# Performance work log

Measured on AMD Instinct MI355X. Metric: run time of the kernel, lower is better.

Reference implementation:

```python
import jax, jax.numpy as jnp
import numpy as np

N = 50000      # num nodes
E = 800000     # num edges
IN_DIM = 128
OUT_DIM = 128
HEADS = 4
HEAD_DIM = OUT_DIM // HEADS  # concat=True
TAU = 1.0


def setup_inputs() -> dict:
    key = jax.random.key(0)
    ks = jax.random.split(key, 8)
    x = jax.random.normal(ks[0], (N, IN_DIM), dtype=jnp.float32)
    edge_index = jax.random.randint(ks[1], (2, E), 0, N, dtype=jnp.int64)
    # xavier-uniform-ish linear weights, stored as (in, out) so y = x @ W
    def xavier(k, fan_in, fan_out):
        limit = np.sqrt(6.0 / (fan_in + fan_out)).astype(np.float32)
        return jax.random.uniform(k, (fan_in, fan_out), jnp.float32, -limit, limit)
    Wt = xavier(ks[2], IN_DIM, HEADS * HEAD_DIM)
    Ws = xavier(ks[3], IN_DIM, HEADS * HEAD_DIM)
    Wc = xavier(ks[4], IN_DIM, HEADS * HEAD_DIM)
    Wout = xavier(ks[5], HEADS * HEAD_DIM, OUT_DIM)
    bout = jnp.zeros((OUT_DIM,), jnp.float32)
    return {"x": x, "edge_index": edge_index, "Wt": Wt, "Ws": Ws,
            "Wc": Wc, "Wout": Wout, "bout": bout}


def reference(x, edge_index, Wt, Ws, Wc, Wout, bout):
    src = edge_index[0]  # j (source of message)
    dst = edge_index[1]  # i (target, softmax group)
    q = (x @ Wt).reshape(N, HEADS, HEAD_DIM)
    k = (x @ Ws).reshape(N, HEADS, HEAD_DIM)
    v = (x @ Wc).reshape(N, HEADS, HEAD_DIM)
    # per-edge dot-product scores: (E, H)
    scores = jnp.einsum('ehd,ehd->eh', q[dst], k[src]) / TAU
    # segment softmax over incoming edges of each dst node
    m = jax.ops.segment_max(scores, dst, num_segments=N)        # (N, H)
    e = jnp.exp(scores - m[dst])                                # (E, H)
    denom = jax.ops.segment_sum(e, dst, num_segments=N)         # (N, H)
    alpha = e / denom[dst]                                      # (E, H)
    # weighted scatter-add aggregation
    msg = v[src] * alpha[:, :, None]                            # (E, H, D)
    agg = jax.ops.segment_sum(msg, dst, num_segments=N)         # (N, H, D)
    out = agg.reshape(N, HEADS * HEAD_DIM) @ Wout + bout
    out = jax.nn.relu(out)
    # residual: in_dim == out_dim -> identity projection
    return out + x
```

## Files before the change

kernel.cpp:

```cpp
#include <hip/hip_runtime.h>
#include <hip/hip_bf16.h>

#define HEADS 4
#define HEAD_DIM 32
#define SLAB 128

typedef __bf16 bf16x8 __attribute__((ext_vector_type(8)));
typedef float  f32x4  __attribute__((ext_vector_type(4)));
typedef _Float16 h2   __attribute__((ext_vector_type(2)));

__device__ __forceinline__ unsigned short f2bf(float f) {
    unsigned u = __float_as_uint(f);
    u += 0x7fffu + ((u >> 16) & 1u);
    return (unsigned short)(u >> 16);
}
__device__ __forceinline__ unsigned pack2bf(float a, float b) {
    return (unsigned)f2bf(a) | ((unsigned)f2bf(b) << 16);
}
__device__ __forceinline__ unsigned short f2h(float f) {
    _Float16 h = (_Float16)f;
    return *(unsigned short*)&h;
}

__global__ __launch_bounds__(256) void fillw_kernel(
    const float* __restrict__ W0, const float* __restrict__ W1,
    const float* __restrict__ W2, const float* __restrict__ W3,
    unsigned short* __restrict__ Wsw,
    const int* __restrict__ edge, int E,
    int* __restrict__ cnt, int* __restrict__ col)
{
    if (blockIdx.x < 32) {
        const float* Wm[4] = { W0, W1, W2, W3 };
        int mi = blockIdx.x >> 3;
        const float* __restrict__ W = Wm[mi];
        unsigned short* __restrict__ o = Wsw + (size_t)mi * 16384;
        int t = (blockIdx.x & 7) * 256 + threadIdx.x;
        int kg = t >> 7;
        int n  = t & 127;
        ushort4 p0, p1;
        p0.x = f2bf(W[(kg * 8 + 0) * 128 + n]);
        p0.y = f2bf(W[(kg * 8 + 1) * 128 + n]);
        p0.z = f2bf(W[(kg * 8 + 2) * 128 + n]);
        p0.w = f2bf(W[(kg * 8 + 3) * 128 + n]);
        p1.x = f2bf(W[(kg * 8 + 4) * 128 + n]);
        p1.y = f2bf(W[(kg * 8 + 5) * 128 + n]);
        p1.z = f2bf(W[(kg * 8 + 6) * 128 + n]);
        p1.w = f2bf(W[(kg * 8 + 7) * 128 + n]);
        *(ushort4*)(o + kg * 1024 + n * 8)     = p0;
        *(ushort4*)(o + kg * 1024 + n * 8 + 4) = p1;
    } else {
        int e = (blockIdx.x - 32) * 256 + threadIdx.x;
        if (e < E) {
            int dst = edge[E + e];
            int src = edge[e];
            int pos = atomicAdd(&cnt[dst], 1);
            if (pos < SLAB)
                col[(size_t)dst * SLAB + pos] = src;
        }
    }
}

__device__ __forceinline__ void mfma_compute64g(
    const unsigned short* As, const unsigned short* __restrict__ Bsw,
    f32x4 (&acc)[2][4], int mb, int nb, int quad, int l16)
{
    #pragma unroll
    for (int a = 0; a < 2; a++)
        #pragma unroll
        for (int b = 0; b < 4; b++)
            #pragma unroll
            for (int e = 0; e < 4; e++) acc[a][b][e] = 0.f;

    #pragma unroll
    for (int kk = 0; kk < 4; kk++) {
        bf16x8 af[2], bf[4];
        #pragma unroll
        for (int mt = 0; mt < 2; mt++)
            af[mt] = *(const bf16x8*)(As + (mb + mt * 16 + l16) * 136
                                         + kk * 32 + quad * 8);
        #pragma unroll
        for (int nt = 0; nt < 4; nt++)
            bf[nt] = *(const bf16x8*)(Bsw + (kk * 4 + quad) * 1024
                                          + (nb + nt * 16 + l16) * 8);
        #pragma unroll
        for (int mt = 0; mt < 2; mt++)
            #pragma unroll
            for (int nt = 0; nt < 4; nt++)
                acc[mt][nt] = __builtin_amdgcn_mfma_f32_16x16x32_bf16(
                    af[mt], bf[nt], acc[mt][nt], 0, 0, 0);
    }
}

__global__ __launch_bounds__(256) void qkv_kernel(
    const float* __restrict__ x, const unsigned short* __restrict__ Wsw,
    unsigned short* __restrict__ qh, unsigned short* __restrict__ kh,
    unsigned short* __restrict__ vh, int M)
{
    __shared__ __align__(16) unsigned short As[64 * 136];
    const int r0 = blockIdx.x * 64;
    const int t  = threadIdx.x;

    #pragma unroll
    for (int it = 0; it < 4; it++) {
        int c   = t + it * 256;
        int row = c >> 4, kp = c & 15;
        float4 a = make_float4(0.f, 0.f, 0.f, 0.f);
        float4 b = make_float4(0.f, 0.f, 0.f, 0.f);
        if (r0 + row < M) {
            a = *(const float4*)(x + (size_t)(r0 + row) * 128 + kp * 8);
            b = *(const float4*)(x + (size_t)(r0 + row) * 128 + kp * 8 + 4);
        }
        uint4 pk;
        pk.x = pack2bf(a.x, a.y);
        pk.y = pack2bf(a.z, a.w);
        pk.z = pack2bf(b.x, b.y);
        pk.w = pack2bf(b.z, b.w);
        *(uint4*)(As + row * 136 + kp * 8) = pk;
    }
    __syncthreads();

    const int wave = t >> 6, L = t & 63;
    const int quad = L >> 4, l16 = L & 15;
    const int mb = (wave >> 1) * 32;
    const int nb = (wave & 1) * 64;

    #pragma unroll
    for (int mode = 0; mode < 3; mode++) {
        f32x4 acc[2][4];
        mfma_compute64g(As, Wsw + (size_t)mode * 16384, acc, mb, nb, quad, l16);

        unsigned short* ob = (mode == 0) ? qh : (mode == 1) ? kh : vh;
        #pragma unroll
        for (int mt = 0; mt < 2; mt++) {
            #pragma unroll
            for (int nt = 0; nt < 4; nt++) {
                int colj = nb + nt * 16 + l16;
                #pragma unroll
                for (int r = 0; r < 4; r++) {
                    int row = r0 + mb + mt * 16 + quad * 4 + r;
                    if (row < M)
                        ob[(size_t)row * 128 + colj] = f2h(acc[mt][nt][r]);
                }
            }
        }
    }
}

__global__ __launch_bounds__(256) void out_mfma_kernel(
    const unsigned short* __restrict__ aggh, const unsigned short* __restrict__ Wsw,
    const float* __restrict__ bout, const float* __restrict__ x,
    float* __restrict__ out, int M)
{
    __shared__ __align__(16) unsigned short As[64 * 136];
    const int r0 = blockIdx.x * 64;
    const int t  = threadIdx.x;

    #pragma unroll
    for (int it = 0; it < 4; it++) {
        int c   = t + it * 256;
        int row = c >> 4, kp = c & 15;
        uint4 val = make_uint4(0, 0, 0, 0);
        if (r0 + row < M)
            val = *(const uint4*)(aggh + (size_t)(r0 + row) * 128 + kp * 8);
        *(uint4*)(As + row * 136 + kp * 8) = val;
    }
    __syncthreads();

    const int wave = t >> 6, L = t & 63;
    const int quad = L >> 4, l16 = L & 15;
    const int mb = (wave >> 1) * 32;
    const int nb = (wave & 1) * 64;

    f32x4 acc[2][4];
    mfma_compute64g(As, Wsw, acc, mb, nb, quad, l16);

    #pragma unroll
    for (int mt = 0; mt < 2; mt++) {
        #pragma unroll
        for (int nt = 0; nt < 4; nt++) {
            int colj = nb + nt * 16 + l16;
            float b = bout[colj];
            #pragma unroll
            for (int r = 0; r < 4; r++) {
                int row = r0 + mb + mt * 16 + quad * 4 + r;
                if (row < M) {
                    float val = fmaxf(acc[mt][nt][r] + b, 0.f)
                              + x[(size_t)row * 128 + colj];
                    out[(size_t)row * 128 + colj] = val;
                }
            }
        }
    }
}

__global__ __launch_bounds__(256, 8) void attn_kernel(
    const unsigned short* __restrict__ qhB, const unsigned short* __restrict__ kh,
    const unsigned short* __restrict__ vh,
    const int* __restrict__ cnt, const int* __restrict__ col,
    unsigned short* __restrict__ aggh, int N)
{
    const int wv   = threadIdx.x >> 6;
    const int lane = threadIdx.x & 63;
    const int dst  = blockIdx.x * 4 + wv;
    if (dst >= N) return;

    __shared__ __align__(16) unsigned short kbuf[4][16 * 136];
    __shared__ __align__(16) float swW[4][64];

    const size_t orow = (size_t)dst * 128;
    const size_t slab = (size_t)dst * SLAB;

    const int h    = lane & 3;
    const int eo   = lane >> 2;
    const int hv   = lane >> 4;
    const int rr   = lane >> 4;
    const int cseg = (lane & 15) * 8;

    const int degr = cnt[dst];
    const int colv = col[slab + lane];
    uint4 qreg[4];
    {
        const uint4* qp = (const uint4*)(qhB + orow + h * HEAD_DIM);
        qreg[0] = qp[0]; qreg[1] = qp[1]; qreg[2] = qp[2]; qreg[3] = qp[3];
    }
    const h2* qv = (const h2*)qreg;

    const int deg = min(degr, SLAB);
    if (deg == 0) {
        *(unsigned*)(aggh + orow + 2 * lane) = 0u;
        return;
    }
    const int srcA = (lane < deg) ? colv : 0;
    int srcB = 0;
    if (__builtin_expect(deg > 64, 0)) {
        if (64 + lane < deg) srcB = col[slab + 64 + lane];
    }

    float sreg[8];
    #pragma unroll
    for (int c = 0; c < 8; c++) {
        sreg[c] = -3.4e38f;
        if (c * 16 < deg) {
            const int nle  = deg - c * 16;
            const int csrc = (c < 4) ? srcA : srcB;
            const int lsel = (c & 3) * 16;
            #pragma unroll
            for (int i = 0; i < 4; i++) {
                int r  = i * 4 + rr;
                int sr = __shfl(csrc, lsel + r);
                uint4 kv = *(const uint4*)(kh + (size_t)sr * 128 + cseg);
                *(uint4*)(&kbuf[wv][r * 136 + cseg]) = kv;
            }
            if (eo < nle) {
                const unsigned short* kb = &kbuf[wv][eo * 136 + h * 32];
                uint4 u0 = *(const uint4*)(kb);
                uint4 u1 = *(const uint4*)(kb + 8);
                uint4 u2 = *(const uint4*)(kb + 16);
                uint4 u3 = *(const uint4*)(kb + 24);
                const h2* p0 = (const h2*)&u0;
                const h2* p1 = (const h2*)&u1;
                const h2* p2 = (const h2*)&u2;
                const h2* p3 = (const h2*)&u3;
                float a = 0.f;
                #pragma unroll
                for (int j = 0; j < 4; j++) {
#if __has_builtin(__builtin_amdgcn_fdot2)
                    a = __builtin_amdgcn_fdot2(qv[j],      p0[j], a, false);
                    a = __builtin_amdgcn_fdot2(qv[4 + j],  p1[j], a, false);
                    a = __builtin_amdgcn_fdot2(qv[8 + j],  p2[j], a, false);
                    a = __builtin_amdgcn_fdot2(qv[12 + j], p3[j], a, false);
#else
                    h2 w0 = qv[j] * p0[j], w1 = qv[4+j] * p1[j];
                    h2 w2 = qv[8+j] * p2[j], w3 = qv[12+j] * p3[j];
                    a += (float)w0[0] + (float)w0[1] + (float)w1[0] + (float)w1[1]
                       + (float)w2[0] + (float)w2[1] + (float)w3[0] + (float)w3[1];
#endif
                }
                sreg[c] = a;
            }
        }
    }

    float m = sreg[0];
    #pragma unroll
    for (int c = 1; c < 8; c++) m = fmaxf(m, sreg[c]);
    #pragma unroll
    for (int off = 4; off < 64; off <<= 1)
        m = fmaxf(m, __shfl_xor(m, off));

    float dsum = 0.f, acc0 = 0.f, acc1 = 0.f;
    #pragma unroll
    for (int c = 0; c < 8; c++) {
        if (c * 16 < deg) {
            const int nle  = min(16, deg - c * 16);
            const int csrc = (c < 4) ? srcA : srcB;
            const int lsel = (c & 3) * 16;
            float ev = (eo < nle) ? __expf(sreg[c] - m) : 0.f;
            dsum += ev;
            swW[wv][lane] = ev;
            if (nle == 16) {
                #pragma unroll
                for (int j = 0; j < 16; j++) {
                    int   sj = __builtin_amdgcn_readlane(csrc, lsel + j);
                    float w  = swW[wv][j * 4 + hv];
                    const unsigned short* vrow = vh + (size_t)sj * 128;
                    unsigned uv = *(const unsigned*)(vrow + 2 * lane);
                    h2 vvv = __builtin_bit_cast(h2, uv);
                    acc0 = fmaf(w, (float)vvv[0], acc0);
                    acc1 = fmaf(w, (float)vvv[1], acc1);
                }
            } else {
                for (int j = 0; j < nle; j++) {
                    int   sj = __builtin_amdgcn_readlane(csrc, lsel + j);
                    float w  = swW[wv][j * 4 + hv];
                    const unsigned short* vrow = vh + (size_t)sj * 128;
                    unsigned uv = *(const unsigned*)(vrow + 2 * lane);
                    h2 vvv = __builtin_bit_cast(h2, uv);
                    acc0 = fmaf(w, (float)vvv[0], acc0);
                    acc1 = fmaf(w, (float)vvv[1], acc1);
                }
            }
        }
    }

    #pragma unroll
    for (int off = 4; off < 64; off <<= 1)
        dsum += __shfl_xor(dsum, off);
    float d   = __shfl(dsum, hv);
    float inv = __builtin_amdgcn_rcpf(d);
    *(unsigned*)(aggh + orow + 2 * lane) = pack2bf(acc0 * inv, acc1 * inv);
}

extern "C" void kernel_launch(void* const* d_in, const int* in_sizes, int n_in,
                              void* d_out, int out_size, void* d_ws, size_t ws_size,
                              hipStream_t stream)
{
    const float* x    = (const float*)d_in[0];
    const int*   edge = (const int*)d_in[1];
    const float* Wt   = (const float*)d_in[2];
    const float* Ws   = (const float*)d_in[3];
    const float* Wc   = (const float*)d_in[4];
    const float* Wout = (const float*)d_in[5];
    const float* bout = (const float*)d_in[6];
    float* out = (float*)d_out;

    const int N = in_sizes[0] / 128;
    const int E = in_sizes[1] / 2;

    unsigned short* qh   = (unsigned short*)d_ws;
    unsigned short* kh   = qh   + (size_t)N * 128;
    unsigned short* vh   = kh   + (size_t)N * 128;
    unsigned short* aggh = vh   + (size_t)N * 128;
    unsigned short* Wsw  = aggh + (size_t)N * 128;
    int* cnt  = (int*)(Wsw + 4 * 16384);
    int* colb = cnt + ((N + 3) & ~3);

    hipMemsetAsync(cnt, 0, (size_t)N * sizeof(int), stream);

    const int gE   = (E + 255) / 256;
    const int gM64 = (N + 63) / 64;

    fillw_kernel<<<32 + gE, 256, 0, stream>>>(Wt, Ws, Wc, Wout, Wsw,
                                              edge, E, cnt, colb);
    qkv_kernel<<<gM64, 256, 0, stream>>>(x, Wsw, qh, kh, vh, N);
    attn_kernel<<<(N + 3) / 4, 256, 0, stream>>>(qh, kh, vh, cnt, colb, aggh, N);
    out_mfma_kernel<<<gM64, 256, 0, stream>>>(aggh, Wsw + 3 * 16384, bout, x, out, N);
}
```

Measured before the change: 232.5 us.

## Fuse all stages into one persistent kernel with grid barriers

Replaces the memset and four separate kernel launches with a single persistent kernel of 1024 blocks. The stages (weight conversion and count zeroing, CSR slab fill plus QKV GEMM, attention, output GEMM) are separated by atomic-counter grid barriers. The aim is to remove launch overhead and inter-kernel gaps and to overlap the edge bucketing with the QKV projection. In exchange it relies on all 1024 blocks being co-resident, since otherwise the spin barriers deadlock. It also limits attention parallelism to a grid-stride loop with occupancy capped at 4 blocks per CU.

Result: slower. 583.0 us (+150.7%).

```diff
diff --git a/kernel.cpp b/kernel.cpp
--- a/kernel.cpp
+++ b/kernel.cpp
@@ -4,6 +4,7 @@
 #define HEADS 4
 #define HEAD_DIM 32
 #define SLAB 128
+#define NBLK 1024
 
 typedef __bf16 bf16x8 __attribute__((ext_vector_type(8)));
 typedef float  f32x4  __attribute__((ext_vector_type(4)));
@@ -22,42 +23,16 @@
     return *(unsigned short*)&h;
 }
 
-__global__ __launch_bounds__(256) void fillw_kernel(
-    const float* __restrict__ W0, const float* __restrict__ W1,
-    const float* __restrict__ W2, const float* __restrict__ W3,
-    unsigned short* __restrict__ Wsw,
-    const int* __restrict__ edge, int E,
-    int* __restrict__ cnt, int* __restrict__ col)
-{
-    if (blockIdx.x < 32) {
-        const float* Wm[4] = { W0, W1, W2, W3 };
-        int mi = blockIdx.x >> 3;
-        const float* __restrict__ W = Wm[mi];
-        unsigned short* __restrict__ o = Wsw + (size_t)mi * 16384;
-        int t = (blockIdx.x & 7) * 256 + threadIdx.x;
-        int kg = t >> 7;
-        int n  = t & 127;
-        ushort4 p0, p1;
-        p0.x = f2bf(W[(kg * 8 + 0) * 128 + n]);
-        p0.y = f2bf(W[(kg * 8 + 1) * 128 + n]);
-        p0.z = f2bf(W[(kg * 8 + 2) * 128 + n]);
-        p0.w = f2bf(W[(kg * 8 + 3) * 128 + n]);
-        p1.x = f2bf(W[(kg * 8 + 4) * 128 + n]);
-        p1.y = f2bf(W[(kg * 8 + 5) * 128 + n]);
-        p1.z = f2bf(W[(kg * 8 + 6) * 128 + n]);
-        p1.w = f2bf(W[(kg * 8 + 7) * 128 + n]);
-        *(ushort4*)(o + kg * 1024 + n * 8)     = p0;
-        *(ushort4*)(o + kg * 1024 + n * 8 + 4) = p1;
-    } else {
-        int e = (blockIdx.x - 32) * 256 + threadIdx.x;
-        if (e < E) {
-            int dst = edge[E + e];
-            int src = edge[e];
-            int pos = atomicAdd(&cnt[dst], 1);
-            if (pos < SLAB)
-                col[(size_t)dst * SLAB + pos] = src;
-        }
-    }
+__device__ __forceinline__ void grid_bar(int* c, int nb) {
+    __syncthreads();
+    if (threadIdx.x == 0) {
+        __threadfence();
+        atomicAdd(c, 1);
+        while (atomicAdd(c, 0) < nb)
+            __builtin_amdgcn_s_sleep(8);
+        __threadfence();
+    }
+    __syncthreads();
 }
 
 __device__ __forceinline__ void mfma_compute64g(
@@ -91,15 +66,10 @@
     }
 }
 
-__global__ __launch_bounds__(256) void qkv_kernel(
-    const float* __restrict__ x, const unsigned short* __restrict__ Wsw,
-    unsigned short* __restrict__ qh, unsigned short* __restrict__ kh,
-    unsigned short* __restrict__ vh, int M)
-{
-    __shared__ __align__(16) unsigned short As[64 * 136];
-    const int r0 = blockIdx.x * 64;
-    const int t  = threadIdx.x;
-
+__device__ __forceinline__ void stage_x_tile(
+    const float* __restrict__ x, int r0, int M, unsigned short* As)
+{
+    const int t = threadIdx.x;
     #pragma unroll
     for (int it = 0; it < 4; it++) {
         int c   = t + it * 256;
@@ -117,44 +87,12 @@
         pk.w = pack2bf(b.z, b.w);
         *(uint4*)(As + row * 136 + kp * 8) = pk;
     }
-    __syncthreads();
-
-    const int wave = t >> 6, L = t & 63;
-    const int quad = L >> 4, l16 = L & 15;
-    const int mb = (wave >> 1) * 32;
-    const int nb = (wave & 1) * 64;
-
-    #pragma unroll
-    for (int mode = 0; mode < 3; mode++) {
-        f32x4 acc[2][4];
-        mfma_compute64g(As, Wsw + (size_t)mode * 16384, acc, mb, nb, quad, l16);
-
-        unsigned short* ob = (mode == 0) ? qh : (mode == 1) ? kh : vh;
-        #pragma unroll
-        for (int mt = 0; mt < 2; mt++) {
-            #pragma unroll
-            for (int nt = 0; nt < 4; nt++) {
-                int colj = nb + nt * 16 + l16;
-                #pragma unroll
-                for (int r = 0; r < 4; r++) {
-                    int row = r0 + mb + mt * 16 + quad * 4 + r;
-                    if (row < M)
-                        ob[(size_t)row * 128 + colj] = f2h(acc[mt][nt][r]);
-                }
-            }
-        }
-    }
-}
-
-__global__ __launch_bounds__(256) void out_mfma_kernel(
-    const unsigned short* __restrict__ aggh, const unsigned short* __restrict__ Wsw,
-    const float* __restrict__ bout, const float* __restrict__ x,
-    float* __restrict__ out, int M)
-{
-    __shared__ __align__(16) unsigned short As[64 * 136];
-    const int r0 = blockIdx.x * 64;
-    const int t  = threadIdx.x;
-
+}
+
+__device__ __forceinline__ void stage_agg_tile(
+    const unsigned short* __restrict__ aggh, int r0, int M, unsigned short* As)
+{
+    const int t = threadIdx.x;
     #pragma unroll
     for (int it = 0; it < 4; it++) {
         int c   = t + it * 256;
@@ -164,48 +102,18 @@
             val = *(const uint4*)(aggh + (size_t)(r0 + row) * 128 + kp * 8);
         *(uint4*)(As + row * 136 + kp * 8) = val;
     }
-    __syncthreads();
-
-    const int wave = t >> 6, L = t & 63;
-    const int quad = L >> 4, l16 = L & 15;
-    const int mb = (wave >> 1) * 32;
-    const int nb = (wave & 1) * 64;
-
-    f32x4 acc[2][4];
-    mfma_compute64g(As, Wsw, acc, mb, nb, quad, l16);
-
-    #pragma unroll
-    for (int mt = 0; mt < 2; mt++) {
-        #pragma unroll
-        for (int nt = 0; nt < 4; nt++) {
-            int colj = nb + nt * 16 + l16;
-            float b = bout[colj];
-            #pragma unroll
-            for (int r = 0; r < 4; r++) {
-                int row = r0 + mb + mt * 16 + quad * 4 + r;
-                if (row < M) {
-                    float val = fmaxf(acc[mt][nt][r] + b, 0.f)
-                              + x[(size_t)row * 128 + colj];
-                    out[(size_t)row * 128 + colj] = val;
-                }
-            }
-        }
-    }
-}
-
-__global__ __launch_bounds__(256, 8) void attn_kernel(
-    const unsigned short* __restrict__ qhB, const unsigned short* __restrict__ kh,
-    const unsigned short* __restrict__ vh,
+}
+
+__device__ void attn_group(
+    int g, const unsigned short* __restrict__ qhB,
+    const unsigned short* __restrict__ kh, const unsigned short* __restrict__ vh,
     const int* __restrict__ cnt, const int* __restrict__ col,
-    unsigned short* __restrict__ aggh, int N)
-{
-    const int wv   = threadIdx.x >> 6;
+    unsigned short* __restrict__ aggh, int N,
+    unsigned short* kbufw, float* swWw)
+{
     const int lane = threadIdx.x & 63;
-    const int dst  = blockIdx.x * 4 + wv;
+    const int dst  = g * 4 + (threadIdx.x >> 6);
     if (dst >= N) return;
-
-    __shared__ __align__(16) unsigned short kbuf[4][16 * 136];
-    __shared__ __align__(16) float swW[4][64];
 
     const size_t orow = (size_t)dst * 128;
     const size_t slab = (size_t)dst * SLAB;
@@ -249,10 +157,10 @@
                 int r  = i * 4 + rr;
                 int sr = __shfl(csrc, lsel + r);
                 uint4 kv = *(const uint4*)(kh + (size_t)sr * 128 + cseg);
-                *(uint4*)(&kbuf[wv][r * 136 + cseg]) = kv;
+                *(uint4*)(&kbufw[r * 136 + cseg]) = kv;
             }
             if (eo < nle) {
-                const unsigned short* kb = &kbuf[wv][eo * 136 + h * 32];
+                const unsigned short* kb = &kbufw[eo * 136 + h * 32];
                 uint4 u0 = *(const uint4*)(kb);
                 uint4 u1 = *(const uint4*)(kb + 8);
                 uint4 u2 = *(const uint4*)(kb + 16);
@@ -297,14 +205,13 @@
             const int lsel = (c & 3) * 16;
             float ev = (eo < nle) ? __expf(sreg[c] - m) : 0.f;
             dsum += ev;
-            swW[wv][lane] = ev;
+            swWw[lane] = ev;
             if (nle == 16) {
                 #pragma unroll
                 for (int j = 0; j < 16; j++) {
                     int   sj = __builtin_amdgcn_readlane(csrc, lsel + j);
-                    float w  = swW[wv][j * 4 + hv];
-                    const unsigned short* vrow = vh + (size_t)sj * 128;
-                    unsigned uv = *(const unsigned*)(vrow + 2 * lane);
+                    float w  = swWw[j * 4 + hv];
+                    unsigned uv = *(const unsigned*)(vh + (size_t)sj * 128 + 2 * lane);
                     h2 vvv = __builtin_bit_cast(h2, uv);
                     acc0 = fmaf(w, (float)vvv[0], acc0);
                     acc1 = fmaf(w, (float)vvv[1], acc1);
@@ -312,9 +219,8 @@
             } else {
                 for (int j = 0; j < nle; j++) {
                     int   sj = __builtin_amdgcn_readlane(csrc, lsel + j);
-                    float w  = swW[wv][j * 4 + hv];
-                    const unsigned short* vrow = vh + (size_t)sj * 128;
-                    unsigned uv = *(const unsigned*)(vrow + 2 * lane);
+                    float w  = swWw[j * 4 + hv];
+                    unsigned uv = *(const unsigned*)(vh + (size_t)sj * 128 + 2 * lane);
                     h2 vvv = __builtin_bit_cast(h2, uv);
                     acc0 = fmaf(w, (float)vvv[0], acc0);
                     acc1 = fmaf(w, (float)vvv[1], acc1);
@@ -329,6 +235,122 @@
     float d   = __shfl(dsum, hv);
     float inv = __builtin_amdgcn_rcpf(d);
     *(unsigned*)(aggh + orow + 2 * lane) = pack2bf(acc0 * inv, acc1 * inv);
+}
+
+__global__ __launch_bounds__(256, 4) void mega_kernel(
+    const float* __restrict__ x, const int* __restrict__ edge,
+    const float* __restrict__ W0, const float* __restrict__ W1,
+    const float* __restrict__ W2, const float* __restrict__ W3,
+    const float* __restrict__ bout, float* __restrict__ out,
+    unsigned short* __restrict__ qh, unsigned short* __restrict__ kh,
+    unsigned short* __restrict__ vh, unsigned short* __restrict__ aggh,
+    unsigned short* __restrict__ Wsw, int* __restrict__ cnt,
+    int* __restrict__ col, int* __restrict__ bar, int N, int E)
+{
+    __shared__ __align__(16) unsigned short sh_u16[4 * 16 * 136];
+    __shared__ __align__(16) float          sh_f32[4 * 64];
+
+    const int t    = threadIdx.x;
+    const int gt   = blockIdx.x * 256 + t;
+    const int gsz  = gridDim.x * 256;
+    const int nblk = gridDim.x;
+    const int nt64 = (N + 63) >> 6;
+
+    const int wave = t >> 6, L = t & 63;
+    const int quad = L >> 4, l16 = L & 15;
+    const int mb = (wave >> 1) * 32;
+    const int nb = (wave & 1) * 64;
+
+    for (int i = gt; i < N; i += gsz) cnt[i] = 0;
+    if (gt < 8192) {
+        const float* Wm[4] = { W0, W1, W2, W3 };
+        int mi = gt >> 11;
+        const float* __restrict__ W = Wm[mi];
+        unsigned short* __restrict__ o = Wsw + (size_t)mi * 16384;
+        int tw = gt & 2047;
+        int kg = tw >> 7;
+        int n  = tw & 127;
+        ushort4 p0, p1;
+        p0.x = f2bf(W[(kg * 8 + 0) * 128 + n]);
+        p0.y = f2bf(W[(kg * 8 + 1) * 128 + n]);
+        p0.z = f2bf(W[(kg * 8 + 2) * 128 + n]);
+        p0.w = f2bf(W[(kg * 8 + 3) * 128 + n]);
+        p1.x = f2bf(W[(kg * 8 + 4) * 128 + n]);
+        p1.y = f2bf(W[(kg * 8 + 5) * 128 + n]);
+        p1.z = f2bf(W[(kg * 8 + 6) * 128 + n]);
+        p1.w = f2bf(W[(kg * 8 + 7) * 128 + n]);
+        *(ushort4*)(o + kg * 1024 + n * 8)     = p0;
+        *(ushort4*)(o + kg * 1024 + n * 8 + 4) = p1;
+    }
+    grid_bar(bar + 0, nblk);
+
+    for (int e = gt; e < E; e += gsz) {
+        int dst = edge[E + e];
+        int src = edge[e];
+        int pos = atomicAdd(&cnt[dst], 1);
+        if (pos < SLAB)
+            col[(size_t)dst * SLAB + pos] = src;
+    }
+    for (int vt = blockIdx.x; vt < 3 * nt64; vt += gridDim.x) {
+        const int mode = vt / nt64;
+        const int r0   = (vt - mode * nt64) * 64;
+        __syncthreads();
+        stage_x_tile(x, r0, N, sh_u16);
+        __syncthreads();
+        f32x4 acc[2][4];
+        mfma_compute64g(sh_u16, Wsw + (size_t)mode * 16384, acc, mb, nb, quad, l16);
+        unsigned short* ob = (mode == 0) ? qh : (mode == 1) ? kh : vh;
+        #pragma unroll
+        for (int mt = 0; mt < 2; mt++) {
+            #pragma unroll
+            for (int nt = 0; nt < 4; nt++) {
+                int colj = nb + nt * 16 + l16;
+                #pragma unroll
+                for (int r = 0; r < 4; r++) {
+                    int row = r0 + mb + mt * 16 + quad * 4 + r;
+                    if (row < N)
+                        ob[(size_t)row * 128 + colj] = f2h(acc[mt][nt][r]);
+                }
+            }
+        }
+    }
+    grid_bar(bar + 1, nblk);
+
+    {
+        const int wv = t >> 6;
+        unsigned short* kbufw = sh_u16 + wv * (16 * 136);
+        float*          swWw  = sh_f32 + wv * 64;
+        const int ng = (N + 3) >> 2;
+        for (int g = blockIdx.x; g < ng; g += gridDim.x)
+            attn_group(g, qh, kh, vh, cnt, col, aggh, N, kbufw, swWw);
+    }
+    grid_bar(bar + 2, nblk);
+
+    for (int tile = blockIdx.x; tile < nt64; tile += gridDim.x) {
+        const int r0 = tile * 64;
+        __syncthreads();
+        stage_agg_tile(aggh, r0, N, sh_u16);
+        __syncthreads();
+        f32x4 acc[2][4];
+        mfma_compute64g(sh_u16, Wsw + (size_t)3 * 16384, acc, mb, nb, quad, l16);
+        #pragma unroll
+        for (int mt = 0; mt < 2; mt++) {
+            #pragma unroll
+            for (int nt = 0; nt < 4; nt++) {
+                int colj = nb + nt * 16 + l16;
+                float b = bout[colj];
+                #pragma unroll
+                for (int r = 0; r < 4; r++) {
+                    int row = r0 + mb + mt * 16 + quad * 4 + r;
+                    if (row < N) {
+                        float val = fmaxf(acc[mt][nt][r] + b, 0.f)
+                                  + x[(size_t)row * 128 + colj];
+                        out[(size_t)row * 128 + colj] = val;
+                    }
+                }
+            }
+        }
+    }
 }
 
 extern "C" void kernel_launch(void* const* d_in, const int* in_sizes, int n_in,
@@ -354,15 +376,11 @@
     unsigned short* Wsw  = aggh + (size_t)N * 128;
     int* cnt  = (int*)(Wsw + 4 * 16384);
     int* colb = cnt + ((N + 3) & ~3);
-
-    hipMemsetAsync(cnt, 0, (size_t)N * sizeof(int), stream);
-
-    const int gE   = (E + 255) / 256;
-    const int gM64 = (N + 63) / 64;
-
-    fillw_kernel<<<32 + gE, 256, 0, stream>>>(Wt, Ws, Wc, Wout, Wsw,
-                                              edge, E, cnt, colb);
-    qkv_kernel<<<gM64, 256, 0, stream>>>(x, Wsw, qh, kh, vh, N);
-    attn_kernel<<<(N + 3) / 4, 256, 0, stream>>>(qh, kh, vh, cnt, colb, aggh, N);
-    out_mfma_kernel<<<gM64, 256, 0, stream>>>(aggh, Wsw + 3 * 16384, bout, x, out, N);
-}
+    int* bar  = colb + (size_t)N * SLAB;
+
+    hipMemsetAsync(bar, 0, 3 * sizeof(int), stream);
+
+    mega_kernel<<<NBLK, 256, 0, stream>>>(
+        x, edge, Wt, Ws, Wc, Wout, bout, out,
+        qh, kh, vh, aggh, Wsw, cnt, colb, bar, N, E);
+}
```

## Fuse graph build with QKV projection and attention with output GEMM

Applied to the files above, without the earlier changes.

The four kernels are merged into two. The first kernel builds the CSR slabs, swizzles Wout, and computes the Q/K/V projections, with each block converting the Wt/Ws/Wc weights into shared memory itself instead of reading a pre-swizzled copy. The second kernel has each wave run attention for 16 destination rows and write the results into a shared-memory tile, then applies the output MFMA GEMM with bias, relu and residual, so the aggh round trip through global memory goes away. In exchange, the fused attention kernel has far fewer blocks and much more shared memory per block, which lowers occupancy for a latency-bound gather. Weight conversion is also repeated in every QKV block.

Result: slower. 336.6 us (+44.7%).

```diff
diff --git a/kernel.cpp b/kernel.cpp
--- a/kernel.cpp
+++ b/kernel.cpp
@@ -22,46 +22,8 @@
     return *(unsigned short*)&h;
 }
 
-__global__ __launch_bounds__(256) void fillw_kernel(
-    const float* __restrict__ W0, const float* __restrict__ W1,
-    const float* __restrict__ W2, const float* __restrict__ W3,
-    unsigned short* __restrict__ Wsw,
-    const int* __restrict__ edge, int E,
-    int* __restrict__ cnt, int* __restrict__ col)
-{
-    if (blockIdx.x < 32) {
-        const float* Wm[4] = { W0, W1, W2, W3 };
-        int mi = blockIdx.x >> 3;
-        const float* __restrict__ W = Wm[mi];
-        unsigned short* __restrict__ o = Wsw + (size_t)mi * 16384;
-        int t = (blockIdx.x & 7) * 256 + threadIdx.x;
-        int kg = t >> 7;
-        int n  = t & 127;
-        ushort4 p0, p1;
-        p0.x = f2bf(W[(kg * 8 + 0) * 128 + n]);
-        p0.y = f2bf(W[(kg * 8 + 1) * 128 + n]);
-        p0.z = f2bf(W[(kg * 8 + 2) * 128 + n]);
-        p0.w = f2bf(W[(kg * 8 + 3) * 128 + n]);
-        p1.x = f2bf(W[(kg * 8 + 4) * 128 + n]);
-        p1.y = f2bf(W[(kg * 8 + 5) * 128 + n]);
-        p1.z = f2bf(W[(kg * 8 + 6) * 128 + n]);
-        p1.w = f2bf(W[(kg * 8 + 7) * 128 + n]);
-        *(ushort4*)(o + kg * 1024 + n * 8)     = p0;
-        *(ushort4*)(o + kg * 1024 + n * 8 + 4) = p1;
-    } else {
-        int e = (blockIdx.x - 32) * 256 + threadIdx.x;
-        if (e < E) {
-            int dst = edge[E + e];
-            int src = edge[e];
-            int pos = atomicAdd(&cnt[dst], 1);
-            if (pos < SLAB)
-                col[(size_t)dst * SLAB + pos] = src;
-        }
-    }
-}
-
 __device__ __forceinline__ void mfma_compute64g(
-    const unsigned short* As, const unsigned short* __restrict__ Bsw,
+    const unsigned short* As, const unsigned short* Bsw,
     f32x4 (&acc)[2][4], int mb, int nb, int quad, int l16)
 {
     #pragma unroll
@@ -91,15 +53,10 @@
     }
 }
 
-__global__ __launch_bounds__(256) void qkv_kernel(
-    const float* __restrict__ x, const unsigned short* __restrict__ Wsw,
-    unsigned short* __restrict__ qh, unsigned short* __restrict__ kh,
-    unsigned short* __restrict__ vh, int M)
-{
-    __shared__ __align__(16) unsigned short As[64 * 136];
-    const int r0 = blockIdx.x * 64;
-    const int t  = threadIdx.x;
-
+__device__ __forceinline__ void stage_x_tile(
+    const float* __restrict__ x, int r0, int M, unsigned short* As)
+{
+    const int t = threadIdx.x;
     #pragma unroll
     for (int it = 0; it < 4; it++) {
         int c   = t + it * 256;
@@ -117,17 +74,78 @@
         pk.w = pack2bf(b.z, b.w);
         *(uint4*)(As + row * 136 + kp * 8) = pk;
     }
-    __syncthreads();
+}
+
+__global__ __launch_bounds__(256) void prep_qkv_kernel(
+    const float* __restrict__ x, const int* __restrict__ edge,
+    const float* __restrict__ Wt, const float* __restrict__ Ws,
+    const float* __restrict__ Wc, const float* __restrict__ Wout,
+    unsigned short* __restrict__ Wsw3,
+    unsigned short* __restrict__ qh, unsigned short* __restrict__ kh,
+    unsigned short* __restrict__ vh,
+    int* __restrict__ cnt, int* __restrict__ col, int N, int E)
+{
+    __shared__ __align__(16) unsigned short As[64 * 136];
+    __shared__ __align__(16) unsigned short Bs[16384];
+
+    const int gE  = (E + 255) >> 8;
+    const int t   = threadIdx.x;
+    const int bid = blockIdx.x;
+
+    if (bid < gE) {
+        int e = bid * 256 + t;
+        if (e < E) {
+            int dst = edge[E + e];
+            int src = edge[e];
+            int pos = atomicAdd(&cnt[dst], 1);
+            if (pos < SLAB)
+                col[(size_t)dst * SLAB + pos] = src;
+        }
+        return;
+    }
+    if (bid < gE + 8) {
+        int tg = (bid - gE) * 256 + t;
+        int kg = tg >> 7, n = tg & 127;
+        const float* wp = Wout + kg * 1024 + n;
+        ushort4 p0, p1;
+        p0.x = f2bf(wp[0]);   p0.y = f2bf(wp[128]);
+        p0.z = f2bf(wp[256]); p0.w = f2bf(wp[384]);
+        p1.x = f2bf(wp[512]); p1.y = f2bf(wp[640]);
+        p1.z = f2bf(wp[768]); p1.w = f2bf(wp[896]);
+        *(ushort4*)(Wsw3 + kg * 1024 + n * 8)     = p0;
+        *(ushort4*)(Wsw3 + kg * 1024 + n * 8 + 4) = p1;
+        return;
+    }
+
+    const int r0 = (bid - gE - 8) * 64;
+    stage_x_tile(x, r0, N, As);
 
     const int wave = t >> 6, L = t & 63;
     const int quad = L >> 4, l16 = L & 15;
     const int mb = (wave >> 1) * 32;
     const int nb = (wave & 1) * 64;
 
+    const float* Wm[3] = { Wt, Ws, Wc };
     #pragma unroll
     for (int mode = 0; mode < 3; mode++) {
+        __syncthreads();
+        #pragma unroll
+        for (int it = 0; it < 8; it++) {
+            int tt = t + it * 256;
+            int kg = tt >> 7, n = tt & 127;
+            const float* wp = Wm[mode] + kg * 1024 + n;
+            ushort4 p0, p1;
+            p0.x = f2bf(wp[0]);   p0.y = f2bf(wp[128]);
+            p0.z = f2bf(wp[256]); p0.w = f2bf(wp[384]);
+            p1.x = f2bf(wp[512]); p1.y = f2bf(wp[640]);
+            p1.z = f2bf(wp[768]); p1.w = f2bf(wp[896]);
+            *(ushort4*)(Bs + kg * 1024 + n * 8)     = p0;
+            *(ushort4*)(Bs + kg * 1024 + n * 8 + 4) = p1;
+        }
+        __syncthreads();
+
         f32x4 acc[2][4];
-        mfma_compute64g(As, Wsw + (size_t)mode * 16384, acc, mb, nb, quad, l16);
+        mfma_compute64g(As, Bs, acc, mb, nb, quad, l16);
 
         unsigned short* ob = (mode == 0) ? qh : (mode == 1) ? kh : vh;
         #pragma unroll
@@ -138,7 +156,7 @@
                 #pragma unroll
                 for (int r = 0; r < 4; r++) {
                     int row = r0 + mb + mt * 16 + quad * 4 + r;
-                    if (row < M)
+                    if (row < N)
                         ob[(size_t)row * 128 + colj] = f2h(acc[mt][nt][r]);
                 }
             }
@@ -146,66 +164,13 @@
     }
 }
 
-__global__ __launch_bounds__(256) void out_mfma_kernel(
-    const unsigned short* __restrict__ aggh, const unsigned short* __restrict__ Wsw,
-    const float* __restrict__ bout, const float* __restrict__ x,
-    float* __restrict__ out, int M)
-{
-    __shared__ __align__(16) unsigned short As[64 * 136];
-    const int r0 = blockIdx.x * 64;
-    const int t  = threadIdx.x;
-
-    #pragma unroll
-    for (int it = 0; it < 4; it++) {
-        int c   = t + it * 256;
-        int row = c >> 4, kp = c & 15;
-        uint4 val = make_uint4(0, 0, 0, 0);
-        if (r0 + row < M)
-            val = *(const uint4*)(aggh + (size_t)(r0 + row) * 128 + kp * 8);
-        *(uint4*)(As + row * 136 + kp * 8) = val;
-    }
-    __syncthreads();
-
-    const int wave = t >> 6, L = t & 63;
-    const int quad = L >> 4, l16 = L & 15;
-    const int mb = (wave >> 1) * 32;
-    const int nb = (wave & 1) * 64;
-
-    f32x4 acc[2][4];
-    mfma_compute64g(As, Wsw, acc, mb, nb, quad, l16);
-
-    #pragma unroll
-    for (int mt = 0; mt < 2; mt++) {
-        #pragma unroll
-        for (int nt = 0; nt < 4; nt++) {
-            int colj = nb + nt * 16 + l16;
-            float b = bout[colj];
-            #pragma unroll
-            for (int r = 0; r < 4; r++) {
-                int row = r0 + mb + mt * 16 + quad * 4 + r;
-                if (row < M) {
-                    float val = fmaxf(acc[mt][nt][r] + b, 0.f)
-                              + x[(size_t)row * 128 + colj];
-                    out[(size_t)row * 128 + colj] = val;
-                }
-            }
-        }
-    }
-}
-
-__global__ __launch_bounds__(256, 8) void attn_kernel(
-    const unsigned short* __restrict__ qhB, const unsigned short* __restrict__ kh,
-    const unsigned short* __restrict__ vh,
+__device__ __forceinline__ void attn_into_lds(
+    int dst, int N, const unsigned short* __restrict__ qhB,
+    const unsigned short* __restrict__ kh, const unsigned short* __restrict__ vh,
     const int* __restrict__ cnt, const int* __restrict__ col,
-    unsigned short* __restrict__ aggh, int N)
-{
-    const int wv   = threadIdx.x >> 6;
-    const int lane = threadIdx.x & 63;
-    const int dst  = blockIdx.x * 4 + wv;
+    unsigned short* kbufw, float* swWw, unsigned short* orowp, int lane)
+{
     if (dst >= N) return;
-
-    __shared__ __align__(16) unsigned short kbuf[4][16 * 136];
-    __shared__ __align__(16) float swW[4][64];
 
     const size_t orow = (size_t)dst * 128;
     const size_t slab = (size_t)dst * SLAB;
@@ -227,7 +192,7 @@
 
     const int deg = min(degr, SLAB);
     if (deg == 0) {
-        *(unsigned*)(aggh + orow + 2 * lane) = 0u;
+        *(unsigned*)(orowp + 2 * lane) = 0u;
         return;
     }
     const int srcA = (lane < deg) ? colv : 0;
@@ -249,10 +214,10 @@
                 int r  = i * 4 + rr;
                 int sr = __shfl(csrc, lsel + r);
                 uint4 kv = *(const uint4*)(kh + (size_t)sr * 128 + cseg);
-                *(uint4*)(&kbuf[wv][r * 136 + cseg]) = kv;
+                *(uint4*)(&kbufw[r * 136 + cseg]) = kv;
             }
             if (eo < nle) {
-                const unsigned short* kb = &kbuf[wv][eo * 136 + h * 32];
+                const unsigned short* kb = &kbufw[eo * 136 + h * 32];
                 uint4 u0 = *(const uint4*)(kb);
                 uint4 u1 = *(const uint4*)(kb + 8);
                 uint4 u2 = *(const uint4*)(kb + 16);
@@ -297,14 +262,13 @@
             const int lsel = (c & 3) * 16;
             float ev = (eo < nle) ? __expf(sreg[c] - m) : 0.f;
             dsum += ev;
-            swW[wv][lane] = ev;
+            swWw[lane] = ev;
             if (nle == 16) {
                 #pragma unroll
                 for (int j = 0; j < 16; j++) {
                     int   sj = __builtin_amdgcn_readlane(csrc, lsel + j);
-                    float w  = swW[wv][j * 4 + hv];
-                    const unsigned short* vrow = vh + (size_t)sj * 128;
-                    unsigned uv = *(const unsigned*)(vrow + 2 * lane);
+                    float w  = swWw[j * 4 + hv];
+                    unsigned uv = *(const unsigned*)(vh + (size_t)sj * 128 + 2 * lane);
                     h2 vvv = __builtin_bit_cast(h2, uv);
                     acc0 = fmaf(w, (float)vvv[0], acc0);
                     acc1 = fmaf(w, (float)vvv[1], acc1);
@@ -312,9 +276,8 @@
             } else {
                 for (int j = 0; j < nle; j++) {
                     int   sj = __builtin_amdgcn_readlane(csrc, lsel + j);
-                    float w  = swW[wv][j * 4 + hv];
-                    const unsigned short* vrow = vh + (size_t)sj * 128;
-                    unsigned uv = *(const unsigned*)(vrow + 2 * lane);
+                    float w  = swWw[j * 4 + hv];
+                    unsigned uv = *(const unsigned*)(vh + (size_t)sj * 128 + 2 * lane);
                     h2 vvv = __builtin_bit_cast(h2, uv);
                     acc0 = fmaf(w, (float)vvv[0], acc0);
                     acc1 = fmaf(w, (float)vvv[1], acc1);
@@ -328,7 +291,54 @@
         dsum += __shfl_xor(dsum, off);
     float d   = __shfl(dsum, hv);
     float inv = __builtin_amdgcn_rcpf(d);
-    *(unsigned*)(aggh + orow + 2 * lane) = pack2bf(acc0 * inv, acc1 * inv);
+    *(unsigned*)(orowp + 2 * lane) = pack2bf(acc0 * inv, acc1 * inv);
+}
+
+__global__ __launch_bounds__(256) void attn_out_kernel(
+    const unsigned short* __restrict__ qh, const unsigned short* __restrict__ kh,
+    const unsigned short* __restrict__ vh,
+    const int* __restrict__ cnt, const int* __restrict__ col,
+    const unsigned short* __restrict__ Wsw3, const float* __restrict__ bout,
+    const float* __restrict__ x, float* __restrict__ out, int N)
+{
+    __shared__ __align__(16) unsigned short As[64 * 136];
+    __shared__ __align__(16) unsigned short kbuf[4][16 * 136];
+    __shared__ __align__(16) float swW[4][64];
+
+    const int t = threadIdx.x, wv = t >> 6, lane = t & 63;
+    const int r0 = blockIdx.x * 64;
+
+    for (int i = 0; i < 16; i++) {
+        const int row = wv * 16 + i;
+        attn_into_lds(r0 + row, N, qh, kh, vh, cnt, col,
+                      kbuf[wv], swW[wv], &As[row * 136], lane);
+    }
+    __syncthreads();
+
+    const int quad = lane >> 4, l16 = lane & 15;
+    const int mb = (wv >> 1) * 32;
+    const int nb = (wv & 1) * 64;
+
+    f32x4 acc[2][4];
+    mfma_compute64g(As, Wsw3, acc, mb, nb, quad, l16);
+
+    #pragma unroll
+    for (int mt = 0; mt < 2; mt++) {
+        #pragma unroll
+        for (int nt = 0; nt < 4; nt++) {
+            int colj = nb + nt * 16 + l16;
+            float b = bout[colj];
+            #pragma unroll
+            for (int r = 0; r < 4; r++) {
+                int row = r0 + mb + mt * 16 + quad * 4 + r;
+                if (row < N) {
+                    float val = fmaxf(acc[mt][nt][r] + b, 0.f)
+                              + x[(size_t)row * 128 + colj];
+                    out[(size_t)row * 128 + colj] = val;
+                }
+            }
+        }
+    }
 }
 
 extern "C" void kernel_launch(void* const* d_in, const int* in_sizes, int n_in,
@@ -350,9 +360,8 @@
     unsigned short* qh   = (unsigned short*)d_ws;
     unsigned short* kh   = qh   + (size_t)N * 128;
     unsigned short* vh   = kh   + (size_t)N * 128;
-    unsigned short* aggh = vh   + (size_t)N * 128;
-    unsigned short* Wsw  = aggh + (size_t)N * 128;
-    int* cnt  = (int*)(Wsw + 4 * 16384);
+    unsigned short* Wsw3 = vh   + (size_t)N * 128;
+    int* cnt  = (int*)(Wsw3 + 16384);
     int* colb = cnt + ((N + 3) & ~3);
 
     hipMemsetAsync(cnt, 0, (size_t)N * sizeof(int), stream);
@@ -360,9 +369,8 @@
     const int gE   = (E + 255) / 256;
     const int gM64 = (N + 63) / 64;
 
-    fillw_kernel<<<32 + gE, 256, 0, stream>>>(Wt, Ws, Wc, Wout, Wsw,
-                                              edge, E, cnt, colb);
-    qkv_kernel<<<gM64, 256, 0, stream>>>(x, Wsw, qh, kh, vh, N);
-    attn_kernel<<<(N + 3) / 4, 256, 0, stream>>>(qh, kh, vh, cnt, colb, aggh, N);
-    out_mfma_kernel<<<gM64, 256, 0, stream>>>(aggh, Wsw + 3 * 16384, bout, x, out, N);
-}
+    prep_qkv_kernel<<<gE + 8 + gM64, 256, 0, stream>>>(
+        x, edge, Wt, Ws, Wc, Wout, Wsw3, qh, kh, vh, cnt, colb, N, E);
+    attn_out_kernel<<<gM64, 256, 0, stream>>>(
+        qh, kh, vh, cnt, colb, Wsw3, bout, x, out, N);
+}
```

## Partition edge bucketing by XCD with work-stealing and 16-bit column indices

Applied to the files above, without the earlier changes.

Replaces the per-edge global-atomic bucketing with a persistent fill kernel. Each XCD scans all edges via a work-stealing chunk counter and inserts only destinations in its own node range, using workgroup-scope atomics. Source indices are stored as 16-bit values, halving column buffer traffic. The goal is to keep atomics local to one XCD's L2 and reduce contention. The cost is that every XCD rereads the edge list, and correctness relies on N fitting in 16 bits and on same-XCD atomic coherence.

New measurement: 371.5 us. 1.6x slower.

```diff
diff --git a/kernel.cpp b/kernel.cpp
--- a/kernel.cpp
+++ b/kernel.cpp
@@ -4,6 +4,7 @@
 #define HEADS 4
 #define HEAD_DIM 32
 #define SLAB 128
+#define NFILL 2048
 
 typedef __bf16 bf16x8 __attribute__((ext_vector_type(8)));
 typedef float  f32x4  __attribute__((ext_vector_type(4)));
@@ -22,46 +23,8 @@
     return *(unsigned short*)&h;
 }
 
-__global__ __launch_bounds__(256) void fillw_kernel(
-    const float* __restrict__ W0, const float* __restrict__ W1,
-    const float* __restrict__ W2, const float* __restrict__ W3,
-    unsigned short* __restrict__ Wsw,
-    const int* __restrict__ edge, int E,
-    int* __restrict__ cnt, int* __restrict__ col)
-{
-    if (blockIdx.x < 32) {
-        const float* Wm[4] = { W0, W1, W2, W3 };
-        int mi = blockIdx.x >> 3;
-        const float* __restrict__ W = Wm[mi];
-        unsigned short* __restrict__ o = Wsw + (size_t)mi * 16384;
-        int t = (blockIdx.x & 7) * 256 + threadIdx.x;
-        int kg = t >> 7;
-        int n  = t & 127;
-        ushort4 p0, p1;
-        p0.x = f2bf(W[(kg * 8 + 0) * 128 + n]);
-        p0.y = f2bf(W[(kg * 8 + 1) * 128 + n]);
-        p0.z = f2bf(W[(kg * 8 + 2) * 128 + n]);
-        p0.w = f2bf(W[(kg * 8 + 3) * 128 + n]);
-        p1.x = f2bf(W[(kg * 8 + 4) * 128 + n]);
-        p1.y = f2bf(W[(kg * 8 + 5) * 128 + n]);
-        p1.z = f2bf(W[(kg * 8 + 6) * 128 + n]);
-        p1.w = f2bf(W[(kg * 8 + 7) * 128 + n]);
-        *(ushort4*)(o + kg * 1024 + n * 8)     = p0;
-        *(ushort4*)(o + kg * 1024 + n * 8 + 4) = p1;
-    } else {
-        int e = (blockIdx.x - 32) * 256 + threadIdx.x;
-        if (e < E) {
-            int dst = edge[E + e];
-            int src = edge[e];
-            int pos = atomicAdd(&cnt[dst], 1);
-            if (pos < SLAB)
-                col[(size_t)dst * SLAB + pos] = src;
-        }
-    }
-}
-
 __device__ __forceinline__ void mfma_compute64g(
-    const unsigned short* As, const unsigned short* __restrict__ Bsw,
+    const unsigned short* As, const unsigned short* Bsw,
     f32x4 (&acc)[2][4], int mb, int nb, int quad, int l16)
 {
     #pragma unroll
@@ -91,15 +54,10 @@
     }
 }
 
-__global__ __launch_bounds__(256) void qkv_kernel(
-    const float* __restrict__ x, const unsigned short* __restrict__ Wsw,
-    unsigned short* __restrict__ qh, unsigned short* __restrict__ kh,
-    unsigned short* __restrict__ vh, int M)
-{
-    __shared__ __align__(16) unsigned short As[64 * 136];
-    const int r0 = blockIdx.x * 64;
-    const int t  = threadIdx.x;
-
+__device__ __forceinline__ void stage_x_tile(
+    const float* __restrict__ x, int r0, int M, unsigned short* As)
+{
+    const int t = threadIdx.x;
     #pragma unroll
     for (int it = 0; it < 4; it++) {
         int c   = t + it * 256;
@@ -117,6 +75,87 @@
         pk.w = pack2bf(b.z, b.w);
         *(uint4*)(As + row * 136 + kp * 8) = pk;
     }
+}
+
+__device__ __forceinline__ void stage_agg_tile(
+    const unsigned short* __restrict__ aggh, int r0, int M, unsigned short* As)
+{
+    const int t = threadIdx.x;
+    #pragma unroll
+    for (int it = 0; it < 4; it++) {
+        int c   = t + it * 256;
+        int row = c >> 4, kp = c & 15;
+        uint4 val = make_uint4(0, 0, 0, 0);
+        if (r0 + row < M)
+            val = *(const uint4*)(aggh + (size_t)(r0 + row) * 128 + kp * 8);
+        *(uint4*)(As + row * 136 + kp * 8) = val;
+    }
+}
+
+__global__ __launch_bounds__(256) void fill_kernel(
+    const int* __restrict__ edge,
+    const float* __restrict__ W0, const float* __restrict__ W1,
+    const float* __restrict__ W2, const float* __restrict__ W3,
+    unsigned short* __restrict__ Wsw,
+    int* __restrict__ cnt, unsigned short* __restrict__ colb,
+    int* __restrict__ wsteal, int N, int E)
+{
+    if (blockIdx.x < 32) {
+        const float* Wm[4] = { W0, W1, W2, W3 };
+        int mi = blockIdx.x >> 3;
+        const float* __restrict__ W = Wm[mi];
+        unsigned short* __restrict__ o = Wsw + (size_t)mi * 16384;
+        int tg = (blockIdx.x & 7) * 256 + threadIdx.x;
+        int kg = tg >> 7, n = tg & 127;
+        const float* wp = W + kg * 1024 + n;
+        ushort4 p0, p1;
+        p0.x = f2bf(wp[0]);   p0.y = f2bf(wp[128]);
+        p0.z = f2bf(wp[256]); p0.w = f2bf(wp[384]);
+        p1.x = f2bf(wp[512]); p1.y = f2bf(wp[640]);
+        p1.z = f2bf(wp[768]); p1.w = f2bf(wp[896]);
+        *(ushort4*)(o + kg * 1024 + n * 8)     = p0;
+        *(ushort4*)(o + kg * 1024 + n * 8 + 4) = p1;
+    }
+
+    int xcd;
+    asm volatile("s_getreg_b32 %0, hwreg(HW_REG_XCC_ID)" : "=s"(xcd));
+    xcd &= 7;
+
+    const int lane = threadIdx.x & 63;
+    const int rng  = (N + 7) >> 3;
+    const int lo   = xcd * rng;
+    const int hi   = min(N, lo + rng);
+    const int nch  = (E + 1023) >> 10;
+
+    for (;;) {
+        int c = 0;
+        if (lane == 0) c = atomicAdd(&wsteal[xcd], 1);
+        c = __shfl(c, 0);
+        if (c >= nch) break;
+        const int e0 = c << 10;
+        const int e1 = min(E, e0 + 1024);
+        for (int e = e0 + lane; e < e1; e += 64) {
+            int dst = __builtin_nontemporal_load(edge + E + e);
+            int src = __builtin_nontemporal_load(edge + e);
+            if (dst >= lo && dst < hi) {
+                int pos = __hip_atomic_fetch_add(&cnt[dst], 1,
+                              __ATOMIC_RELAXED, __HIP_MEMORY_SCOPE_WORKGROUP);
+                if (pos < SLAB)
+                    colb[(size_t)dst * SLAB + pos] = (unsigned short)src;
+            }
+        }
+    }
+}
+
+__global__ __launch_bounds__(256) void qkv_kernel(
+    const float* __restrict__ x, const unsigned short* __restrict__ Wsw,
+    unsigned short* __restrict__ qh, unsigned short* __restrict__ kh,
+    unsigned short* __restrict__ vh, int M)
+{
+    __shared__ __align__(16) unsigned short As[64 * 136];
+    const int r0 = blockIdx.x * 64;
+    const int t  = threadIdx.x;
+    stage_x_tile(x, r0, M, As);
     __syncthreads();
 
     const int wave = t >> 6, L = t & 63;
@@ -128,7 +167,6 @@
     for (int mode = 0; mode < 3; mode++) {
         f32x4 acc[2][4];
         mfma_compute64g(As, Wsw + (size_t)mode * 16384, acc, mb, nb, quad, l16);
-
         unsigned short* ob = (mode == 0) ? qh : (mode == 1) ? kh : vh;
         #pragma unroll
         for (int mt = 0; mt < 2; mt++) {
@@ -146,57 +184,10 @@
     }
 }
 
-__global__ __launch_bounds__(256) void out_mfma_kernel(
-    const unsigned short* __restrict__ aggh, const unsigned short* __restrict__ Wsw,
-    const float* __restrict__ bout, const float* __restrict__ x,
-    float* __restrict__ out, int M)
-{
-    __shared__ __align__(16) unsigned short As[64 * 136];
-    const int r0 = blockIdx.x * 64;
-    const int t  = threadIdx.x;
-
-    #pragma unroll
-    for (int it = 0; it < 4; it++) {
-        int c   = t + it * 256;
-        int row = c >> 4, kp = c & 15;
-        uint4 val = make_uint4(0, 0, 0, 0);
-        if (r0 + row < M)
-            val = *(const uint4*)(aggh + (size_t)(r0 + row) * 128 + kp * 8);
-        *(uint4*)(As + row * 136 + kp * 8) = val;
-    }
-    __syncthreads();
-
-    const int wave = t >> 6, L = t & 63;
-    const int quad = L >> 4, l16 = L & 15;
-    const int mb = (wave >> 1) * 32;
-    const int nb = (wave & 1) * 64;
-
-    f32x4 acc[2][4];
-    mfma_compute64g(As, Wsw, acc, mb, nb, quad, l16);
-
-    #pragma unroll
-    for (int mt = 0; mt < 2; mt++) {
-        #pragma unroll
-        for (int nt = 0; nt < 4; nt++) {
-            int colj = nb + nt * 16 + l16;
-            float b = bout[colj];
-            #pragma unroll
-            for (int r = 0; r < 4; r++) {
-                int row = r0 + mb + mt * 16 + quad * 4 + r;
-                if (row < M) {
-                    float val = fmaxf(acc[mt][nt][r] + b, 0.f)
-                              + x[(size_t)row * 128 + colj];
-                    out[(size_t)row * 128 + colj] = val;
-                }
-            }
-        }
-    }
-}
-
 __global__ __launch_bounds__(256, 8) void attn_kernel(
     const unsigned short* __restrict__ qhB, const unsigned short* __restrict__ kh,
     const unsigned short* __restrict__ vh,
-    const int* __restrict__ cnt, const int* __restrict__ col,
+    const int* __restrict__ cnt, const unsigned short* __restrict__ col,
     unsigned short* __restrict__ aggh, int N)
 {
     const int wv   = threadIdx.x >> 6;
@@ -303,8 +294,7 @@
                 for (int j = 0; j < 16; j++) {
                     int   sj = __builtin_amdgcn_readlane(csrc, lsel + j);
                     float w  = swW[wv][j * 4 + hv];
-                    const unsigned short* vrow = vh + (size_t)sj * 128;
-                    unsigned uv = *(const unsigned*)(vrow + 2 * lane);
+                    unsigned uv = *(const unsigned*)(vh + (size_t)sj * 128 + 2 * lane);
                     h2 vvv = __builtin_bit_cast(h2, uv);
                     acc0 = fmaf(w, (float)vvv[0], acc0);
                     acc1 = fmaf(w, (float)vvv[1], acc1);
@@ -313,8 +303,7 @@
                 for (int j = 0; j < nle; j++) {
                     int   sj = __builtin_amdgcn_readlane(csrc, lsel + j);
                     float w  = swW[wv][j * 4 + hv];
-                    const unsigned short* vrow = vh + (size_t)sj * 128;
-                    unsigned uv = *(const unsigned*)(vrow + 2 * lane);
+                    unsigned uv = *(const unsigned*)(vh + (size_t)sj * 128 + 2 * lane);
                     h2 vvv = __builtin_bit_cast(h2, uv);
                     acc0 = fmaf(w, (float)vvv[0], acc0);
                     acc1 = fmaf(w, (float)vvv[1], acc1);
@@ -329,6 +318,44 @@
     float d   = __shfl(dsum, hv);
     float inv = __builtin_amdgcn_rcpf(d);
     *(unsigned*)(aggh + orow + 2 * lane) = pack2bf(acc0 * inv, acc1 * inv);
+}
+
+__global__ __launch_bounds__(256) void out_mfma_kernel(
+    const unsigned short* __restrict__ aggh, const unsigned short* __restrict__ Wsw3,
+    const float* __restrict__ bout, const float* __restrict__ x,
+    float* __restrict__ out, int M)
+{
+    __shared__ __align__(16) unsigned short As[64 * 136];
+    const int r0 = blockIdx.x * 64;
+    const int t  = threadIdx.x;
+    stage_agg_tile(aggh, r0, M, As);
+    __syncthreads();
+
+    const int wave = t >> 6, L = t & 63;
+    const int quad = L >> 4, l16 = L & 15;
+    const int mb = (wave >> 1) * 32;
+    const int nb = (wave & 1) * 64;
+
+    f32x4 acc[2][4];
+    mfma_compute64g(As, Wsw3, acc, mb, nb, quad, l16);
+
+    #pragma unroll
+    for (int mt = 0; mt < 2; mt++) {
+        #pragma unroll
+        for (int nt = 0; nt < 4; nt++) {
+            int colj = nb + nt * 16 + l16;
+            float b = bout[colj];
+            #pragma unroll
+            for (int r = 0; r < 4; r++) {
+                int row = r0 + mb + mt * 16 + quad * 4 + r;
+                if (row < M) {
+                    float val = fmaxf(acc[mt][nt][r] + b, 0.f)
+                              + x[(size_t)row * 128 + colj];
+                    out[(size_t)row * 128 + colj] = val;
+                }
+            }
+        }
+    }
 }
 
 extern "C" void kernel_launch(void* const* d_in, const int* in_sizes, int n_in,
@@ -352,17 +379,20 @@
     unsigned short* vh   = kh   + (size_t)N * 128;
     unsigned short* aggh = vh   + (size_t)N * 128;
     unsigned short* Wsw  = aggh + (size_t)N * 128;
-    int* cnt  = (int*)(Wsw + 4 * 16384);
-    int* colb = cnt + ((N + 3) & ~3);
-
-    hipMemsetAsync(cnt, 0, (size_t)N * sizeof(int), stream);
-
-    const int gE   = (E + 255) / 256;
+    unsigned short* colb = Wsw  + 4 * 16384;
+    const int cntpad = (N + 3) & ~3;
+    int* cnt    = (int*)(colb + (size_t)N * SLAB);
+    int* wsteal = cnt + cntpad;
+
+    hipMemsetAsync(cnt, 0, (size_t)(cntpad + 8) * sizeof(int), stream);
+
     const int gM64 = (N + 63) / 64;
 
-    fillw_kernel<<<32 + gE, 256, 0, stream>>>(Wt, Ws, Wc, Wout, Wsw,
-                                              edge, E, cnt, colb);
+    fill_kernel<<<NFILL, 256, 0, stream>>>(
+        edge, Wt, Ws, Wc, Wout, Wsw, cnt, colb, wsteal, N, E);
     qkv_kernel<<<gM64, 256, 0, stream>>>(x, Wsw, qh, kh, vh, N);
-    attn_kernel<<<(N + 3) / 4, 256, 0, stream>>>(qh, kh, vh, cnt, colb, aggh, N);
-    out_mfma_kernel<<<gM64, 256, 0, stream>>>(aggh, Wsw + 3 * 16384, bout, x, out, N);
-}
+    attn_kernel<<<(N + 3) / 4, 256, 0, stream>>>(
+        qh, kh, vh, cnt, colb, aggh, N);
+    out_mfma_kernel<<<gM64, 256, 0, stream>>>(
+        aggh, Wsw + 3 * 16384, bout, x, out, N);
+}
```
